# Kernel tuning notes

Measured on AMD Instinct MI355X. Metric: run time of the kernel, lower is better.

Reference implementation:

```python
import jax, jax.numpy as jnp
import numpy as np

B, T, DM, H, HD = 2, 2048, 1024, 16, 64

def _rope_cos_sin(t, hd):
    inv_freq = 1.0 / (10000.0 ** (jnp.arange(0, hd, 2, dtype=jnp.float32) / hd))
    ang = jnp.arange(t, dtype=jnp.float32)[:, None] * inv_freq[None, :]  # [T, hd/2]
    emb = jnp.concatenate([ang, ang], axis=-1)  # [T, hd]
    return jnp.cos(emb), jnp.sin(emb)

def setup_inputs() -> dict:
    key = jax.random.key(0)
    kx, kq, kp = jax.random.split(key, 3)
    x = jax.random.normal(kx, (B, T, DM), dtype=jnp.float32)
    cos, sin = _rope_cos_sin(T, HD)
    w_qkv = jax.random.normal(kq, (3 * DM, DM), dtype=jnp.float32) * (DM ** -0.5)
    w_proj = jax.random.normal(kp, (DM, DM), dtype=jnp.float32) * (DM ** -0.5)
    return {"x": x, "cos": cos, "sin": sin, "w_qkv": w_qkv, "w_proj": w_proj}

def _rotate_half(u):
    d = u.shape[-1] // 2
    return jnp.concatenate([-u[..., d:], u[..., :d]], axis=-1)

def _apply_rope(u, cos, sin):
    # u: [B, T, H, D]; cos/sin: [T, D] -> unsqueeze_dim=1 -> [T, 1, D]
    c = cos[:, None, :]
    s = sin[:, None, :]
    return u * c + _rotate_half(u) * s

def reference(x, cos, sin, w_qkv, w_proj):
    b, t, _ = x.shape
    qkv = jnp.einsum('btd,ed->bte', x, w_qkv)            # [B, T, 3*DM]
    qkv = qkv.reshape(b, t, 3, H, HD)
    q, k, v = qkv[:, :, 0], qkv[:, :, 1], qkv[:, :, 2]   # each [B, T, H, HD]
    q = _apply_rope(q, cos, sin)
    k = _apply_rope(k, cos, sin)
    q = q.transpose(0, 2, 1, 3)                          # [B, H, T, HD]
    k = k.transpose(0, 2, 1, 3)
    v = v.transpose(0, 2, 1, 3)
    scale = 1.0 / jnp.sqrt(jnp.float32(HD))
    scores = jnp.einsum('bhqd,bhkd->bhqk', q, k) * scale  # [B, H, T, T]
    causal = jnp.tril(jnp.ones((t, t), dtype=bool))
    scores = jnp.where(causal[None, None], scores, jnp.finfo(scores.dtype).min)
    attn = jax.nn.softmax(scores, axis=-1)
    out = jnp.einsum('bhqk,bhkd->bhqd', attn, v)          # [B, H, T, HD]
    out = out.transpose(0, 2, 1, 3).reshape(b, t, H * HD)
    return jnp.einsum('btd,ed->bte', out, w_proj)
```

## Files before the change

kernel.cpp:

```cpp
#include <hip/hip_runtime.h>
#include <stdint.h>

#define Bb 2
#define Tt 2048
#define DMm 1024
#define Hh 16
#define HDd 64
#define Mrows (Bb*Tt)

typedef __attribute__((ext_vector_type(8)))  __bf16 bf16x8;
typedef __attribute__((ext_vector_type(4)))  __bf16 bf16x4;
typedef __attribute__((ext_vector_type(4)))  float  f32x4;
typedef __attribute__((ext_vector_type(16))) float  f32x16;
typedef __attribute__((ext_vector_type(4)))  unsigned int u32x4;
typedef __attribute__((ext_vector_type(2)))  unsigned int u32x2;

#define GLD16(gp, lp) __builtin_amdgcn_global_load_lds( \
    (const __attribute__((address_space(1))) unsigned int*)(gp), \
    (__attribute__((address_space(3))) unsigned int*)(lp), 16, 0, 0)

static __device__ __forceinline__ unsigned cvtpk_bf16(float lo, float hi) {
  unsigned r;
  asm("v_cvt_pk_bf16_f32 %0, %1, %2" : "=v"(r) : "v"(lo), "v"(hi));
  return r;
}
static __device__ __forceinline__ float exp2_hw(float x) {
  float r;
  asm("v_exp_f32 %0, %1" : "=v"(r) : "v"(x));
  return r;
}
static __device__ __forceinline__ float xmax32(float v) {
  return fmaxf(v, __shfl_xor(v, 32));
}
static __device__ __forceinline__ float xsum32(float v) {
  return v + __shfl_xor(v, 32);
}

__global__ __launch_bounds__(256)
void cast3_k(const float* __restrict__ a, const float* __restrict__ b,
             const float* __restrict__ c,
             __bf16* __restrict__ oa, __bf16* __restrict__ ob,
             __bf16* __restrict__ oc,
             const float* __restrict__ cosb, const float* __restrict__ sinb,
             unsigned* __restrict__ cs) {
  const int NA = 1048576, NB = 786432, NC = 262144;
  int i = blockIdx.x * 256 + threadIdx.x;
  if (i < NA + NB + NC) {
    const float* src; __bf16* dst; int k;
    if (i < NA)            { src = a; dst = oa; k = i; }
    else if (i < NA + NB)  { src = b; dst = ob; k = i - NA; }
    else                   { src = c; dst = oc; k = i - NA - NB; }
    float4 v = ((const float4*)src)[k];
    bf16x4 o;
    o[0] = (__bf16)v.x; o[1] = (__bf16)v.y; o[2] = (__bf16)v.z; o[3] = (__bf16)v.w;
    ((bf16x4*)dst)[k] = o;
  } else {
    int k = i - (NA + NB + NC);
    cs[k] = cvtpk_bf16(cosb[k], sinb[k]);
  }
}

__global__ __launch_bounds__(256)
void gemm_bt(const __bf16* __restrict__ A, const __bf16* __restrict__ Bm,
             float* __restrict__ C, int M, int N, int K) {
  __shared__ __bf16 As[128 * 32];
  __shared__ __bf16 Bs[128 * 32];
  const int tid  = threadIdx.x;
  const int lane = tid & 63, wid = tid >> 6;
  const int l4 = lane & 15, lhi = lane >> 4;
  const int rowBase = blockIdx.y * 128, colBase = blockIdx.x * 128;
  const int wh = wid >> 1, ww = wid & 1;
  f32x4 acc[4][4] = {};
  const int e0 = wid * 512 + lane * 8;
  const int r0 = e0 >> 5, c0 = e0 & 31;
  const __bf16* a0 = A  + (size_t)(rowBase + r0)      * K + c0;
  const __bf16* a1 = A  + (size_t)(rowBase + r0 + 64) * K + c0;
  const __bf16* b0 = Bm + (size_t)(colBase + r0)      * K + c0;
  const __bf16* b1 = Bm + (size_t)(colBase + r0 + 64) * K + c0;
  for (int k0 = 0; k0 < K; k0 += 32) {
    __syncthreads();
    GLD16(a0 + k0, &As[wid * 512]);
    GLD16(a1 + k0, &As[2048 + wid * 512]);
    GLD16(b0 + k0, &Bs[wid * 512]);
    GLD16(b1 + k0, &Bs[2048 + wid * 512]);
    __syncthreads();
    bf16x8 af[4], bfr[4];
#pragma unroll
    for (int i = 0; i < 4; i++) {
      af[i]  = *(const bf16x8*)&As[(wh * 64 + i * 16 + l4) * 32 + lhi * 8];
      bfr[i] = *(const bf16x8*)&Bs[(ww * 64 + i * 16 + l4) * 32 + lhi * 8];
    }
#pragma unroll
    for (int i = 0; i < 4; i++)
#pragma unroll
      for (int j = 0; j < 4; j++)
        acc[i][j] = __builtin_amdgcn_mfma_f32_16x16x32_bf16(af[i], bfr[j], acc[i][j], 0, 0, 0);
  }
#pragma unroll
  for (int i = 0; i < 4; i++) {
    int R = rowBase + wh * 64 + i * 16 + lhi * 4;
#pragma unroll
    for (int j = 0; j < 4; j++) {
      int Cc = colBase + ww * 64 + j * 16 + l4;
      float* cp = C + (size_t)R * N + Cc;
#pragma unroll
      for (int q = 0; q < 4; q++) cp[(size_t)q * N] = acc[i][j][q];
    }
  }
}

__global__ __launch_bounds__(256)
void gemm_qkv(const __bf16* __restrict__ A, const __bf16* __restrict__ Bm,
              __bf16* __restrict__ Qb, __bf16* __restrict__ Kb,
              __bf16* __restrict__ Vfb, const unsigned* __restrict__ csb) {
  const int K = 1024;
  __shared__ __bf16 ldsu[16384];
  __bf16* As = ldsu;
  __bf16* Bs = ldsu + 4096;
  const int tid  = threadIdx.x;
  const int lane = tid & 63, wid = tid >> 6;
  const int l4 = lane & 15, lhi = lane >> 4;
  const int rowBase = blockIdx.y * 128, colBase = blockIdx.x * 128;
  const int wh = wid >> 1, ww = wid & 1;
  f32x4 acc[4][4] = {};
  const int e0 = wid * 512 + lane * 8;
  const int r0 = e0 >> 5, c0 = e0 & 31;
  const __bf16* a0 = A  + (size_t)(rowBase + r0)      * K + c0;
  const __bf16* a1 = A  + (size_t)(rowBase + r0 + 64) * K + c0;
  const __bf16* b0 = Bm + (size_t)(colBase + r0)      * K + c0;
  const __bf16* b1 = Bm + (size_t)(colBase + r0 + 64) * K + c0;
  for (int k0 = 0; k0 < K; k0 += 32) {
    __syncthreads();
    GLD16(a0 + k0, &As[wid * 512]);
    GLD16(a1 + k0, &As[2048 + wid * 512]);
    GLD16(b0 + k0, &Bs[wid * 512]);
    GLD16(b1 + k0, &Bs[2048 + wid * 512]);
    __syncthreads();
    bf16x8 af[4], bfr[4];
#pragma unroll
    for (int i = 0; i < 4; i++) {
      af[i]  = *(const bf16x8*)&As[(wh * 64 + i * 16 + l4) * 32 + lhi * 8];
      bfr[i] = *(const bf16x8*)&Bs[(ww * 64 + i * 16 + l4) * 32 + lhi * 8];
    }
#pragma unroll
    for (int i = 0; i < 4; i++)
#pragma unroll
      for (int j = 0; j < 4; j++)
        acc[i][j] = __builtin_amdgcn_mfma_f32_16x16x32_bf16(af[i], bfr[j], acc[i][j], 0, 0, 0);
  }

  const int region = colBase >> 10;
  const int base_h = (colBase & 1023) >> 6;
  const int bIdx   = rowBase >> 11;
  const int tileBase = (rowBase & 2047) >> 5;

  __syncthreads();

  if (region < 2) {
    const float qscale = region ? 1.f : 0.18033688f;
#pragma unroll
    for (int i = 0; i < 4; i++) {
      const int tbase = ww * 8192 + (wh * 2 + (i >> 1)) * 2048;
      const int rsub  = (i & 1) * 16 + lhi * 4;
      const int trow0 = (rowBase & 2047) + wh * 64 + i * 16 + lhi * 4;
#pragma unroll
      for (int j = 0; j < 4; j++) {
        int dd = j * 16 + l4;
        float sg = (j < 2) ? -1.f : 1.f;
        int lbase = tbase + j * 512 + (l4 >> 3) * 256 + (l4 & 7);
#pragma unroll
        for (int q = 0; q < 4; q++) {
          unsigned cw = csb[(trow0 + q) * 64 + dd];
          float cc = __builtin_bit_cast(float, cw << 16);
          float sn = __builtin_bit_cast(float, cw & 0xffff0000u);
          float r = (acc[i][j][q] * cc + sg * acc[i][j ^ 2][q] * sn) * qscale;
          ldsu[lbase + (rsub + q) * 8] = (__bf16)r;
        }
      }
    }
  } else {
#pragma unroll
    for (int i = 0; i < 4; i++) {
      const int tbase = ww * 8192 + (wh * 2 + (i >> 1)) * 2048 + (i & 1) * 512;
#pragma unroll
      for (int j = 0; j < 4; j++) {
        int lbase = tbase + (j >> 1) * 1024 + ((j & 1) * 16 + l4) * 8;
#pragma unroll
        for (int q = 0; q < 4; q++) {
          int rq = lhi * 4 + q;
          ldsu[lbase + ((rq >> 3) & 1) * 256 + (rq & 7)] = (__bf16)acc[i][j][q];
        }
      }
    }
  }
  __syncthreads();

  __bf16* dstBuf = (region == 0) ? Qb : (region == 1 ? Kb : Vfb);
#pragma unroll
  for (int h2 = 0; h2 < 2; ++h2) {
    __bf16* dst = dstBuf + (size_t)(bIdx * 16 + base_h + h2) * (Tt * 64)
                + (size_t)tileBase * 2048;
#pragma unroll
    for (int k = 0; k < 4; ++k) {
      int eoff = k * 2048 + tid * 8;
      *(bf16x8*)(dst + eoff) = *(const bf16x8*)&ldsu[h2 * 8192 + eoff];
    }
  }
}

__global__ __launch_bounds__(256)
void attn_k(const __bf16* __restrict__ Q, const __bf16* __restrict__ K,
            const __bf16* __restrict__ Vb, __bf16* __restrict__ O) {
  const int bid = blockIdx.x;
  const int xcd = bid & 7;
  const int ii  = bid >> 3;
  const int bh  = xcd * 4 + (ii & 3);
  const int jj  = ii >> 2;
  const int b = bh >> 4, h = bh & 15;
  const int tid = threadIdx.x, lane = tid & 63, w = tid >> 6;
  const int l5 = lane & 31, hi = lane >> 5;
  const size_t baseF = (size_t)bh * (Tt * 64);
  const int laneoff = (hi << 8) + (l5 << 3);
  const float NEG_INF = -__builtin_inff();

  __shared__ float  oL[4][32][65];
  __shared__ float2 msL[4][32];

#define FRAGP(P, tile, c) ((P) + baseF + (size_t)(((tile) * 4 + (c)) << 9) + laneoff)

#define LOADK(KA, TIX) do {                                               \
    KA[0] = *(const bf16x8*)FRAGP(K, (TIX), 0);                           \
    KA[1] = *(const bf16x8*)FRAGP(K, (TIX), 1);                           \
    KA[2] = *(const bf16x8*)FRAGP(K, (TIX), 2);                           \
    KA[3] = *(const bf16x8*)FRAGP(K, (TIX), 3);                           \
  } while (0)
#define LOADV(TIX) do {                                                   \
    vc[0] = *(const bf16x8*)FRAGP(Vb, (TIX), 0);                          \
    vc[1] = *(const bf16x8*)FRAGP(Vb, (TIX), 1);                          \
    vc[2] = *(const bf16x8*)FRAGP(Vb, (TIX), 2);                          \
    vc[3] = *(const bf16x8*)FRAGP(Vb, (TIX), 3);                          \
  } while (0)

#define COMPUTE(KA, TIX) do {                                             \
    f32x16 s = {};                                                        \
    __builtin_amdgcn_s_setprio(1);                                        \
    s = __builtin_amdgcn_mfma_f32_32x32x16_bf16(KA[0], qf[0], s, 0, 0, 0);\
    s = __builtin_amdgcn_mfma_f32_32x32x16_bf16(KA[1], qf[1], s, 0, 0, 0);\
    s = __builtin_amdgcn_mfma_f32_32x32x16_bf16(KA[2], qf[2], s, 0, 0, 0);\
    s = __builtin_amdgcn_mfma_f32_32x32x16_bf16(KA[3], qf[3], s, 0, 0, 0);\
    __builtin_amdgcn_s_setprio(0);                                        \
    float sv[16];                                                         \
    if ((TIX) == qsub) {                                                  \
      _Pragma("unroll")                                                   \
      for (int r = 0; r < 16; r++) {                                      \
        int kof = (r & 3) + 8 * (r >> 2) + 4 * hi;                        \
        sv[r] = (kof <= l5) ? s[r] : NEG_INF;                             \
      }                                                                   \
    } else {                                                              \
      _Pragma("unroll")                                                   \
      for (int r = 0; r < 16; r++) sv[r] = s[r];                          \
    }                                                                     \
    float pmax = sv[0];                                                   \
    _Pragma("unroll")                                                     \
    for (int r = 1; r < 16; r++) pmax = fmaxf(pmax, sv[r]);               \
    pmax = xmax32(pmax);                                                  \
    if (__any(pmax > m + 11.5f)) {                                        \
      float mn = fmaxf(m, pmax);                                          \
      float al = exp2_hw(m - mn);                                         \
      m = mn;                                                             \
      ssum *= al;                                                         \
      float arow[16];                                                     \
      _Pragma("unroll")                                                   \
      for (int r = 0; r < 16; r++)                                        \
        arow[r] = __shfl(al, (r & 3) + 8 * (r >> 2) + 4 * hi);            \
      _Pragma("unroll")                                                   \
      for (int r = 0; r < 16; r++) { o0[r] *= arow[r]; o1[r] *= arow[r]; }\
    }                                                                     \
    float p[16], rsl = 0.f;                                               \
    _Pragma("unroll")                                                     \
    for (int r = 0; r < 16; r++) { p[r] = exp2_hw(sv[r] - m); rsl += p[r]; } \
    ssum += xsum32(rsl);                                                  \
    bf16x8 pa[2];                                                         \
    _Pragma("unroll")                                                     \
    for (int kc = 0; kc < 2; kc++) {                                      \
      const float* pp = p + kc * 8;                                       \
      unsigned X0 = cvtpk_bf16(pp[0], pp[1]);                             \
      unsigned Y0 = cvtpk_bf16(pp[4], pp[5]);                             \
      unsigned X1 = cvtpk_bf16(pp[2], pp[3]);                             \
      unsigned Y1 = cvtpk_bf16(pp[6], pp[7]);                             \
      u32x2 q0 = __builtin_amdgcn_permlane32_swap(X0, Y0, false, false);  \
      u32x2 q1 = __builtin_amdgcn_permlane32_swap(X1, Y1, false, false);  \
      u32x4 pw;                                                           \
      pw[0] = q0[0]; pw[1] = q1[0]; pw[2] = q0[1]; pw[3] = q1[1];         \
      pa[kc] = __builtin_bit_cast(bf16x8, pw);                            \
    }                                                                     \
    __builtin_amdgcn_s_setprio(1);                                        \
    o0 = __builtin_amdgcn_mfma_f32_32x32x16_bf16(pa[0], vc[0], o0, 0, 0, 0);\
    o0 = __builtin_amdgcn_mfma_f32_32x32x16_bf16(pa[1], vc[1], o0, 0, 0, 0);\
    o1 = __builtin_amdgcn_mfma_f32_32x32x16_bf16(pa[0], vc[2], o1, 0, 0, 0);\
    o1 = __builtin_amdgcn_mfma_f32_32x32x16_bf16(pa[1], vc[3], o1, 0, 0, 0);\
    __builtin_amdgcn_s_setprio(0);                                        \
  } while (0)

#define TCLAMP(tx) ( ((tx) > qsub) ? qsub : (tx) )

  for (int ph = 0; ph < 2; ++ph) {
    const int qsub  = ph ? (63 - jj) : jj;
    const int qrow0 = qsub * 32;

    bf16x8 qf[4];
#pragma unroll
    for (int cc = 0; cc < 4; cc++)
      qf[cc] = *(const bf16x8*)FRAGP(Q, qsub, cc);

    f32x16 o0 = {}, o1 = {};
    float m = NEG_INF, ssum = 0.f;

    const int NT = qsub + 1;
    const int dtw = NT - w;
    const int n = (dtw > 0) ? ((dtw + 3) >> 2) : 0;

    bf16x8 kA[4], kB[4], vc[4];

    LOADK(kA, TCLAMP(w));
    int i = 0;
    for (; i + 2 <= n; i += 2) {
      LOADV(w + 4 * i);
      LOADK(kB, TCLAMP(w + 4 * i + 4));
      COMPUTE(kA, w + 4 * i);
      LOADV(w + 4 * i + 4);
      LOADK(kA, TCLAMP(w + 4 * i + 8));
      COMPUTE(kB, w + 4 * i + 4);
    }
    if (i < n) {
      LOADV(w + 4 * i);
      COMPUTE(kA, w + 4 * i);
    }

#pragma unroll
    for (int r = 0; r < 16; r++) {
      int row = (r & 3) + 8 * (r >> 2) + 4 * hi;
      oL[w][row][l5]      = o0[r];
      oL[w][row][32 + l5] = o1[r];
    }
    if (hi == 0) msL[w][l5] = make_float2(m, ssum);
    __syncthreads();

    {
      const int row = l5;
      const int dbase = w * 16 + hi * 8;
      float2 s0 = msL[0][row], s1 = msL[1][row], s2 = msL[2][row], s3 = msL[3][row];
      float M = fmaxf(fmaxf(s0.x, s1.x), fmaxf(s2.x, s3.x));
      float a0 = exp2_hw(s0.x - M), a1 = exp2_hw(s1.x - M);
      float a2 = exp2_hw(s2.x - M), a3 = exp2_hw(s3.x - M);
      float inv = 1.f / (a0 * s0.y + a1 * s1.y + a2 * s2.y + a3 * s3.y);
      bf16x8 ov;
#pragma unroll
      for (int e = 0; e < 8; e++) {
        float v = a0 * oL[0][row][dbase + e] + a1 * oL[1][row][dbase + e]
                + a2 * oL[2][row][dbase + e] + a3 * oL[3][row][dbase + e];
        ov[e] = (__bf16)(v * inv);
      }
      *(bf16x8*)(O + ((size_t)b * Tt + qrow0 + row) * DMm + h * 64 + dbase) = ov;
    }
    __syncthreads();
  }
}

extern "C" void kernel_launch(void* const* d_in, const int* in_sizes, int n_in,
                              void* d_out, int out_size, void* d_ws, size_t ws_size,
                              hipStream_t stream) {
  const float* x     = (const float*)d_in[0];
  const float* cosb  = (const float*)d_in[1];
  const float* sinb  = (const float*)d_in[2];
  const float* wqkv  = (const float*)d_in[3];
  const float* wproj = (const float*)d_in[4];
  float* out = (float*)d_out;

  char* ws = (char*)d_ws;
  __bf16*   xb     = (__bf16*)(ws + 0);
  __bf16*   wqkvb  = (__bf16*)(ws + 8388608);
  __bf16*   wprojb = (__bf16*)(ws + 14680064);
  unsigned* csb    = (unsigned*)(ws + 16777216);
  __bf16*   Qb     = (__bf16*)(ws + 17825792);
  __bf16*   Kb     = (__bf16*)(ws + 26214400);
  __bf16*   Vfb    = (__bf16*)(ws + 34603008);
  __bf16*   attno  = (__bf16*)(ws + 42991616);

  cast3_k<<<8704, 256, 0, stream>>>(x, wqkv, wproj, xb, wqkvb, wprojb,
                                    cosb, sinb, csb);

  dim3 g1(3072 / 128, Mrows / 128);
  gemm_qkv<<<g1, 256, 0, stream>>>(xb, wqkvb, Qb, Kb, Vfb, csb);

  attn_k<<<1024, 256, 0, stream>>>(Qb, Kb, Vfb, attno);

  dim3 g2(DMm / 128, Mrows / 128);
  gemm_bt<<<g2, 256, 0, stream>>>(attno, wprojb, out, Mrows, DMm, 1024);
}
```

Baseline: 110.8 us.

## Remap GEMM blocks per XCD, shrink proj GEMM tile, use max3 in softmax

Both GEMMs now launch on a 1D grid whose block index is remapped so that consecutive blocks landing on the same XCD share row panels, which should improve L2 reuse of the A operand. The output-projection GEMM also drops to a 128x64 tile, doubling its block count from 256 to 512 so more CUs are busy. The attention softmax masks in place and reduces the row max with a three-input max tree instead of a linear chain. The smaller tile reads the A operand more times, and the XCD mapping assumes round-robin dispatch of blocks across 8 XCDs.

```diff
diff --git a/kernel.cpp b/kernel.cpp
--- a/kernel.cpp
+++ b/kernel.cpp
@@ -28,6 +28,9 @@
   float r;
   asm("v_exp_f32 %0, %1" : "=v"(r) : "v"(x));
   return r;
+}
+static __device__ __forceinline__ float fmax3(float a, float b, float c) {
+  return fmaxf(fmaxf(a, b), c);
 }
 static __device__ __forceinline__ float xmax32(float v) {
   return fmaxf(v, __shfl_xor(v, 32));
@@ -62,46 +65,49 @@
 
 __global__ __launch_bounds__(256)
 void gemm_bt(const __bf16* __restrict__ A, const __bf16* __restrict__ Bm,
-             float* __restrict__ C, int M, int N, int K) {
+             float* __restrict__ C) {
+  const int N = 1024, K = 1024;
   __shared__ __bf16 As[128 * 32];
-  __shared__ __bf16 Bs[128 * 32];
+  __shared__ __bf16 Bs[64 * 32];
+  const int bid = blockIdx.x;
+  const int xcd = bid & 7, i2 = bid >> 3;
+  const int rowBase = (xcd * 4 + (i2 & 3)) * 128;
+  const int colBase = (i2 >> 2) * 64;
   const int tid  = threadIdx.x;
   const int lane = tid & 63, wid = tid >> 6;
   const int l4 = lane & 15, lhi = lane >> 4;
-  const int rowBase = blockIdx.y * 128, colBase = blockIdx.x * 128;
   const int wh = wid >> 1, ww = wid & 1;
-  f32x4 acc[4][4] = {};
+  f32x4 acc[4][2] = {};
   const int e0 = wid * 512 + lane * 8;
   const int r0 = e0 >> 5, c0 = e0 & 31;
   const __bf16* a0 = A  + (size_t)(rowBase + r0)      * K + c0;
   const __bf16* a1 = A  + (size_t)(rowBase + r0 + 64) * K + c0;
   const __bf16* b0 = Bm + (size_t)(colBase + r0)      * K + c0;
-  const __bf16* b1 = Bm + (size_t)(colBase + r0 + 64) * K + c0;
   for (int k0 = 0; k0 < K; k0 += 32) {
     __syncthreads();
     GLD16(a0 + k0, &As[wid * 512]);
     GLD16(a1 + k0, &As[2048 + wid * 512]);
     GLD16(b0 + k0, &Bs[wid * 512]);
-    GLD16(b1 + k0, &Bs[2048 + wid * 512]);
-    __syncthreads();
-    bf16x8 af[4], bfr[4];
-#pragma unroll
-    for (int i = 0; i < 4; i++) {
+    __syncthreads();
+    bf16x8 af[4], bfr[2];
+#pragma unroll
+    for (int i = 0; i < 4; i++)
       af[i]  = *(const bf16x8*)&As[(wh * 64 + i * 16 + l4) * 32 + lhi * 8];
-      bfr[i] = *(const bf16x8*)&Bs[(ww * 64 + i * 16 + l4) * 32 + lhi * 8];
-    }
+#pragma unroll
+    for (int j = 0; j < 2; j++)
+      bfr[j] = *(const bf16x8*)&Bs[(ww * 32 + j * 16 + l4) * 32 + lhi * 8];
 #pragma unroll
     for (int i = 0; i < 4; i++)
 #pragma unroll
-      for (int j = 0; j < 4; j++)
+      for (int j = 0; j < 2; j++)
         acc[i][j] = __builtin_amdgcn_mfma_f32_16x16x32_bf16(af[i], bfr[j], acc[i][j], 0, 0, 0);
   }
 #pragma unroll
   for (int i = 0; i < 4; i++) {
     int R = rowBase + wh * 64 + i * 16 + lhi * 4;
 #pragma unroll
-    for (int j = 0; j < 4; j++) {
-      int Cc = colBase + ww * 64 + j * 16 + l4;
+    for (int j = 0; j < 2; j++) {
+      int Cc = colBase + ww * 32 + j * 16 + l4;
       float* cp = C + (size_t)R * N + Cc;
 #pragma unroll
       for (int q = 0; q < 4; q++) cp[(size_t)q * N] = acc[i][j][q];
@@ -117,10 +123,13 @@
   __shared__ __bf16 ldsu[16384];
   __bf16* As = ldsu;
   __bf16* Bs = ldsu + 4096;
+  const int bid = blockIdx.x;
+  const int xcd = bid & 7, i2 = bid >> 3;
+  const int rowBase = (xcd * 4 + (i2 & 3)) * 128;
+  const int colBase = (i2 >> 2) * 128;
   const int tid  = threadIdx.x;
   const int lane = tid & 63, wid = tid >> 6;
   const int l4 = lane & 15, lhi = lane >> 4;
-  const int rowBase = blockIdx.y * 128, colBase = blockIdx.x * 128;
   const int wh = wid >> 1, ww = wid & 1;
   f32x4 acc[4][4] = {};
   const int e0 = wid * 512 + lane * 8;
@@ -249,20 +258,19 @@
     s = __builtin_amdgcn_mfma_f32_32x32x16_bf16(KA[2], qf[2], s, 0, 0, 0);\
     s = __builtin_amdgcn_mfma_f32_32x32x16_bf16(KA[3], qf[3], s, 0, 0, 0);\
     __builtin_amdgcn_s_setprio(0);                                        \
-    float sv[16];                                                         \
     if ((TIX) == qsub) {                                                  \
       _Pragma("unroll")                                                   \
       for (int r = 0; r < 16; r++) {                                      \
         int kof = (r & 3) + 8 * (r >> 2) + 4 * hi;                        \
-        sv[r] = (kof <= l5) ? s[r] : NEG_INF;                             \
+        s[r] = (kof <= l5) ? s[r] : NEG_INF;                              \
       }                                                                   \
-    } else {                                                              \
-      _Pragma("unroll")                                                   \
-      for (int r = 0; r < 16; r++) sv[r] = s[r];                          \
     }                                                                     \
-    float pmax = sv[0];                                                   \
-    _Pragma("unroll")                                                     \
-    for (int r = 1; r < 16; r++) pmax = fmaxf(pmax, sv[r]);               \
+    float t0 = fmax3(s[0], s[1], s[2]);                                   \
+    float t1 = fmax3(s[3], s[4], s[5]);                                   \
+    float t2 = fmax3(s[6], s[7], s[8]);                                   \
+    float t3 = fmax3(s[9], s[10], s[11]);                                 \
+    float t4 = fmax3(s[12], s[13], s[14]);                                \
+    float pmax = fmaxf(fmax3(t0, t1, t2), fmax3(t3, t4, s[15]));          \
     pmax = xmax32(pmax);                                                  \
     if (__any(pmax > m + 11.5f)) {                                        \
       float mn = fmaxf(m, pmax);                                          \
@@ -278,7 +286,7 @@
     }                                                                     \
     float p[16], rsl = 0.f;                                               \
     _Pragma("unroll")                                                     \
-    for (int r = 0; r < 16; r++) { p[r] = exp2_hw(sv[r] - m); rsl += p[r]; } \
+    for (int r = 0; r < 16; r++) { p[r] = exp2_hw(s[r] - m); rsl += p[r]; } \
     ssum += xsum32(rsl);                                                  \
     bf16x8 pa[2];                                                         \
     _Pragma("unroll")                                                     \
@@ -390,11 +398,9 @@
   cast3_k<<<8704, 256, 0, stream>>>(x, wqkv, wproj, xb, wqkvb, wprojb,
                                     cosb, sinb, csb);
 
-  dim3 g1(3072 / 128, Mrows / 128);
-  gemm_qkv<<<g1, 256, 0, stream>>>(xb, wqkvb, Qb, Kb, Vfb, csb);
+  gemm_qkv<<<768, 256, 0, stream>>>(xb, wqkvb, Qb, Kb, Vfb, csb);
 
   attn_k<<<1024, 256, 0, stream>>>(Qb, Kb, Vfb, attno);
 
-  dim3 g2(DMm / 128, Mrows / 128);
-  gemm_bt<<<g2, 256, 0, stream>>>(attno, wprojb, out, Mrows, DMm, 1024);
-}
+  gemm_bt<<<512, 256, 0, stream>>>(attno, wprojb, out);
+}
```

Result: faster. 99.19 us, median of 3 (-10.5%).
